# Optimization experiments

Measured on AMD Instinct MI355X. Metric: run time of the kernel, lower is better.

Reference implementation:

```python
import jax, jax.numpy as jnp
import numpy as np

N_NODES = 100_000
N_EDGES = 1_000_000
IN_FTS = 64
EDGE_IN_FTS = 64
OUT_DIM = 64
LN_EPS = 1e-5


def setup_inputs() -> dict:
    key = jax.random.key(0)
    ks = jax.random.split(key, 9)
    def lin(k, fan_in, fan_out):
        bound = 1.0 / np.sqrt(fan_in)
        kw, kb = jax.random.split(k)
        W = jax.random.uniform(kw, (fan_out, fan_in), jnp.float32, -bound, bound)
        b = jax.random.uniform(kb, (fan_out,), jnp.float32, -bound, bound)
        return W, b
    node_fts = jax.random.normal(ks[0], (N_NODES, IN_FTS), jnp.float32)
    edge_fts = jax.random.normal(ks[1], (N_EDGES, EDGE_IN_FTS), jnp.float32)
    edges = jax.random.randint(ks[2], (2, N_EDGES), 0, N_NODES, jnp.int64)
    W_init, b_init = lin(ks[3], EDGE_IN_FTS, OUT_DIM)
    W_mlp, b_mlp = lin(ks[4], 2 * IN_FTS + OUT_DIM, OUT_DIM)
    W_alpha, b_alpha = lin(ks[5], 2 * IN_FTS + OUT_DIM, 1)
    return {
        "node_fts": node_fts, "edge_fts": edge_fts, "edges": edges,
        "W_init": W_init, "b_init": b_init,
        "W_mlp": W_mlp, "b_mlp": b_mlp,
        "W_alpha": W_alpha, "b_alpha": b_alpha,
    }


def _layer_norm(x):
    # F.layer_norm over last dim, no affine params
    m = jnp.mean(x, axis=-1, keepdims=True)
    v = jnp.mean(jnp.square(x - m), axis=-1, keepdims=True)
    return (x - m) * jax.lax.rsqrt(v + LN_EPS)


def reference(node_fts, edge_fts, edges, W_init, b_init, W_mlp, b_mlp, W_alpha, b_alpha):
    # initial edge projection: [E, edge_in] -> [E, out_dim]
    e = edge_fts @ W_init.T + b_init
    # gather head/tail node features: [E, in_fts] each
    head_vectors = jnp.take(node_fts, edges[0], axis=0)
    tail_vectors = jnp.take(node_fts, edges[1], axis=0)
    combined = jnp.concatenate([e, head_vectors, tail_vectors], axis=1)  # [E, 2*in+out]
    alpha = jax.nn.sigmoid(combined @ W_alpha.T + b_alpha)  # [E, 1]
    processed = jnp.tanh(combined @ W_mlp.T + b_mlp)        # [E, out_dim]
    right_side = _layer_norm(processed) * alpha
    return _layer_norm(e + right_side)
```

## Files before the change

kernel.cpp:

```cpp
#include <hip/hip_runtime.h>
#include <hip/hip_bf16.h>

typedef __bf16 bf16;
typedef bf16 bf16x8 __attribute__((ext_vector_type(8)));
typedef float f32x4 __attribute__((ext_vector_type(4)));

#define MFMA16(a, b, c) __builtin_amdgcn_mfma_f32_16x16x32_bf16((a), (b), (c), 0, 0, 0)
#define UNROLL _Pragma("unroll")

__device__ __forceinline__ float fast_rcp(float x) { return __builtin_amdgcn_rcpf(x); }
__device__ __forceinline__ float fast_rsq(float x) { return __builtin_amdgcn_rsqf(x); }
__device__ __forceinline__ float fast_tanh(float x) {
    float e = __expf(2.0f * x);
    return 1.0f - 2.0f * fast_rcp(e + 1.0f);
}
__device__ __forceinline__ float fast_sigmoid(float x) {
    return fast_rcp(1.0f + __expf(-x));
}

__device__ __forceinline__ bf16x8 cvt8(const float* __restrict__ p) {
    f32x4 a = *(const f32x4*)p;
    f32x4 b = *(const f32x4*)(p + 4);
    bf16x8 r;
    r[0] = (bf16)a[0]; r[1] = (bf16)a[1]; r[2] = (bf16)a[2]; r[3] = (bf16)a[3];
    r[4] = (bf16)b[0]; r[5] = (bf16)b[1]; r[6] = (bf16)b[2]; r[7] = (bf16)b[3];
    return r;
}
__device__ __forceinline__ bf16x8 cvt8v(f32x4 a, f32x4 b) {
    bf16x8 r;
    r[0] = (bf16)a[0]; r[1] = (bf16)a[1]; r[2] = (bf16)a[2]; r[3] = (bf16)a[3];
    r[4] = (bf16)b[0]; r[5] = (bf16)b[1]; r[6] = (bf16)b[2]; r[7] = (bf16)b[3];
    return r;
}

template <int CTRL>
__device__ __forceinline__ float dpp_add(float v) {
    int t = __builtin_amdgcn_update_dpp(0, __float_as_int(v), CTRL, 0xF, 0xF, false);
    return v + __int_as_float(t);
}
__device__ __forceinline__ float sum16(float v) {
    v = dpp_add<0x121>(v);
    v = dpp_add<0x122>(v);
    v = dpp_add<0x124>(v);
    v = dpp_add<0x128>(v);
    return v;
}

#define WS_WAF  8192
#define WS_BMF  8320
#define WS_BAF  8576
#define WS_NODE 16384

__global__ void prep_kernel(const float* __restrict__ W_init,
                            const float* __restrict__ b_init,
                            const float* __restrict__ W_mlp,
                            const float* __restrict__ b_mlp,
                            const float* __restrict__ W_alpha,
                            const float* __restrict__ b_alpha,
                            const float* __restrict__ node_fts,
                            char* __restrict__ ws,
                            int nchunks)
{
    const int idx = blockIdx.x * 256 + threadIdx.x;
    if (blockIdx.x < 17) {
        bf16*  Wf  = (bf16*)ws;
        bf16*  waf = (bf16*)(ws + WS_WAF);
        float* bMf = (float*)(ws + WS_BMF);
        float* bAf = (float*)(ws + WS_BAF);
        if (idx < 4096) {
            const int o = idx >> 6, k = idx & 63;
            float acc = 0.f;
            for (int j = 0; j < 64; ++j)
                acc += W_mlp[o * 192 + j] * W_init[j * 64 + k];
            Wf[o * 64 + k] = (bf16)acc;
        } else if (idx < 4160) {
            const int o = idx - 4096;
            float acc = b_mlp[o];
            for (int j = 0; j < 64; ++j)
                acc += W_mlp[o * 192 + j] * b_init[j];
            bMf[o] = acc;
        } else if (idx < 4224) {
            const int k = idx - 4160;
            float acc = 0.f;
            for (int j = 0; j < 64; ++j)
                acc += W_alpha[j] * W_init[j * 64 + k];
            waf[k] = (bf16)acc;
        } else if (idx == 4224) {
            float acc = b_alpha[0];
            for (int j = 0; j < 64; ++j)
                acc += W_alpha[j] * b_init[j];
            bAf[0] = acc;
        }
    } else {
        const int i = idx - 17 * 256;
        if (i < nchunks) {
            bf16* nc = (bf16*)(ws + WS_NODE);
            f32x4 a = *(const f32x4*)(node_fts + (size_t)i * 8);
            f32x4 b = *(const f32x4*)(node_fts + (size_t)i * 8 + 4);
            *(bf16x8*)(nc + (size_t)i * 8) = cvt8v(a, b);
        }
    }
}

#define ISSUE_STAGE(sp, e0s, hs, ts)                                          \
    {                                                                         \
        const float* ep_ = edge_fts + ((size_t)(e0s) + n) * 64;               \
        ef[sp][0] = *(const f32x4*)(ep_ + q * 8);                             \
        ef[sp][1] = *(const f32x4*)(ep_ + q * 8 + 4);                         \
        ef[sp][2] = *(const f32x4*)(ep_ + 32 + q * 8);                        \
        ef[sp][3] = *(const f32x4*)(ep_ + 32 + q * 8 + 4);                    \
        if constexpr (NB) {                                                   \
            const bf16* hp_ = nc + (size_t)(hs) * 64;                         \
            const bf16* tp_ = nc + (size_t)(ts) * 64;                         \
            nhB[sp][0] = *(const bf16x8*)(hp_ + q * 8);                       \
            nhB[sp][1] = *(const bf16x8*)(hp_ + 32 + q * 8);                  \
            ntB[sp][0] = *(const bf16x8*)(tp_ + q * 8);                       \
            ntB[sp][1] = *(const bf16x8*)(tp_ + 32 + q * 8);                  \
        } else {                                                              \
            const float* hp_ = node_fts + (size_t)(hs) * 64;                  \
            const float* tp_ = node_fts + (size_t)(ts) * 64;                  \
            nhF[sp][0] = *(const f32x4*)(hp_ + q * 8);                        \
            nhF[sp][1] = *(const f32x4*)(hp_ + q * 8 + 4);                    \
            nhF[sp][2] = *(const f32x4*)(hp_ + 32 + q * 8);                   \
            nhF[sp][3] = *(const f32x4*)(hp_ + 32 + q * 8 + 4);               \
            ntF[sp][0] = *(const f32x4*)(tp_ + q * 8);                        \
            ntF[sp][1] = *(const f32x4*)(tp_ + q * 8 + 4);                    \
            ntF[sp][2] = *(const f32x4*)(tp_ + 32 + q * 8);                   \
            ntF[sp][3] = *(const f32x4*)(tp_ + 32 + q * 8 + 4);               \
        }                                                                     \
    }

template <bool NB>
__global__ __launch_bounds__(256, 3)
void edge_update_kernel(const float* __restrict__ node_fts,
                        const float* __restrict__ edge_fts,
                        const int*   __restrict__ edges,
                        const float* __restrict__ W_init,
                        const float* __restrict__ b_init,
                        const float* __restrict__ W_mlp,
                        const float* __restrict__ W_alpha,
                        const char*  __restrict__ ws,
                        float* __restrict__ out,
                        int E)
{
    __shared__ bf16 sW2[64][264];
    __shared__ bf16 sWa[224];

    const int tid  = threadIdx.x;
    const int lane = tid & 63;
    const int wv   = tid >> 6;
    const int n    = lane & 15;
    const int q    = lane >> 4;

    const bf16*  Wf  = (const bf16*)ws;
    const bf16*  waf = (const bf16*)(ws + WS_WAF);
    const float* bMf = (const float*)(ws + WS_BMF);
    const float* bAf = (const float*)(ws + WS_BAF);
    const bf16*  nc  = (const bf16*)(ws + WS_NODE);

    for (int c = tid; c < 64 * 33; c += 256) {
        const int r = c / 33;
        const int o = (c - r * 33) * 8;
        if (o < 64)       *(bf16x8*)(&sW2[r][o]) = *(const bf16x8*)(Wf + r * 64 + o);
        else if (o < 192) *(bf16x8*)(&sW2[r][o]) = cvt8(W_mlp + r * 192 + o);
        else if (o < 256) *(bf16x8*)(&sW2[r][o]) = cvt8(W_init + r * 64 + (o - 192));
    }
    if (tid < 24) {
        const int o = tid * 8;
        if (o < 64) *(bf16x8*)(&sWa[o]) = *(const bf16x8*)(waf + o);
        else        *(bf16x8*)(&sWa[o]) = cvt8(W_alpha + o);
    }
    __syncthreads();

    float bI[4], bM[4];
    UNROLL
    for (int t = 0; t < 4; ++t) {
        bI[t] = b_init[t * 16 + n];
        bM[t] = bMf[t * 16 + n];
    }
    const float bA = bAf[0];

    const int ngroups = E >> 4;
    const int stride  = gridDim.x * 4;
    int gc = blockIdx.x * 4 + wv;
    if (gc >= ngroups) return;

    f32x4  ef[2][4];
    bf16x8 nhB[2][2], ntB[2][2];
    f32x4  nhF[2][4], ntF[2][4];

    {
        const int e0 = gc << 4;
        const int hc = edges[e0 + n];
        const int tc = edges[E + e0 + n];
        ISSUE_STAGE(0, e0, hc, tc);
    }
    int gn = gc + stride, hn = 0, tn = 0;
    if (gn < ngroups) {
        const int e0n = gn << 4;
        hn = edges[e0n + n];
        tn = edges[E + e0n + n];
    } else {
        gn = gc;
    }

    for (;;) {
        UNROLL
        for (int p = 0; p < 2; ++p) {
            const int np = p ^ 1;
            const bool haveNext = (gn != gc);
            int g2 = gn;
            if (haveNext) {
                ISSUE_STAGE(np, gn << 4, hn, tn);
                g2 = gn + stride;
                if (g2 < ngroups) {
                    const int e2 = g2 << 4;
                    hn = edges[e2 + n];
                    tn = edges[E + e2 + n];
                } else {
                    g2 = gn;
                }
            }

            const int e0c = gc << 4;
            bf16x8 A[6];
            A[0] = cvt8v(ef[p][0], ef[p][1]);
            A[1] = cvt8v(ef[p][2], ef[p][3]);
            if constexpr (NB) {
                A[2] = nhB[p][0]; A[3] = nhB[p][1];
                A[4] = ntB[p][0]; A[5] = ntB[p][1];
            } else {
                A[2] = cvt8v(nhF[p][0], nhF[p][1]); A[3] = cvt8v(nhF[p][2], nhF[p][3]);
                A[4] = cvt8v(ntF[p][0], ntF[p][1]); A[5] = cvt8v(ntF[p][2], ntF[p][3]);
            }

            f32x4 accE[4] = { f32x4{0,0,0,0}, f32x4{0,0,0,0}, f32x4{0,0,0,0}, f32x4{0,0,0,0} };
            UNROLL
            for (int kk = 0; kk < 2; ++kk)
                UNROLL
                for (int t = 0; t < 4; ++t)
                    accE[t] = MFMA16(A[kk],
                                     *(const bf16x8*)(&sW2[t * 16 + n][192 + kk * 32 + q * 8]),
                                     accE[t]);

            f32x4 accP[4] = { f32x4{0,0,0,0}, f32x4{0,0,0,0}, f32x4{0,0,0,0}, f32x4{0,0,0,0} };
            f32x4 accA = f32x4{0,0,0,0};
            UNROLL
            for (int kk = 0; kk < 6; ++kk) {
                accA = MFMA16(A[kk], *(const bf16x8*)(&sWa[kk * 32 + q * 8]), accA);
                UNROLL
                for (int t = 0; t < 4; ++t)
                    accP[t] = MFMA16(A[kk],
                                     *(const bf16x8*)(&sW2[t * 16 + n][kk * 32 + q * 8]),
                                     accP[t]);
            }

            float eF[4][4], pv[4][4], alpha[4];
            UNROLL
            for (int t = 0; t < 4; ++t)
                UNROLL
                for (int r = 0; r < 4; ++r) eF[t][r] = accE[t][r] + bI[t];
            UNROLL
            for (int r = 0; r < 4; ++r) alpha[r] = fast_sigmoid(accA[r] + bA);
            UNROLL
            for (int t = 0; t < 4; ++t)
                UNROLL
                for (int r = 0; r < 4; ++r) pv[t][r] = fast_tanh(accP[t][r] + bM[t]);

            float s1[4], s2[4];
            UNROLL
            for (int r = 0; r < 4; ++r) {
                s1[r] = pv[0][r] + pv[1][r] + pv[2][r] + pv[3][r];
                s2[r] = pv[0][r]*pv[0][r] + pv[1][r]*pv[1][r] + pv[2][r]*pv[2][r] + pv[3][r]*pv[3][r];
            }
            UNROLL
            for (int r = 0; r < 4; ++r) { s1[r] = sum16(s1[r]); s2[r] = sum16(s2[r]); }

            float o2[4][4];
            UNROLL
            for (int r = 0; r < 4; ++r) {
                const float mean = s1[r] * 0.015625f;
                const float var  = fmaxf(s2[r] * 0.015625f - mean * mean, 0.0f);
                const float rs   = fast_rsq(var + 1e-5f);
                UNROLL
                for (int t = 0; t < 4; ++t)
                    o2[t][r] = eF[t][r] + (pv[t][r] - mean) * rs * alpha[r];
            }

            UNROLL
            for (int r = 0; r < 4; ++r) {
                s1[r] = o2[0][r] + o2[1][r] + o2[2][r] + o2[3][r];
                s2[r] = o2[0][r]*o2[0][r] + o2[1][r]*o2[1][r] + o2[2][r]*o2[2][r] + o2[3][r]*o2[3][r];
            }
            UNROLL
            for (int r = 0; r < 4; ++r) { s1[r] = sum16(s1[r]); s2[r] = sum16(s2[r]); }

            UNROLL
            for (int r = 0; r < 4; ++r) {
                const float mean = s1[r] * 0.015625f;
                const float var  = fmaxf(s2[r] * 0.015625f - mean * mean, 0.0f);
                const float rs   = fast_rsq(var + 1e-5f);
                UNROLL
                for (int t = 0; t < 4; ++t)
                    out[((size_t)e0c + q * 4 + r) * 64 + t * 16 + n] = (o2[t][r] - mean) * rs;
            }

            if (!haveNext) return;
            gc = gn;
            gn = g2;
        }
    }
}

extern "C" void kernel_launch(void* const* d_in, const int* in_sizes, int n_in,
                              void* d_out, int out_size, void* d_ws, size_t ws_size,
                              hipStream_t stream) {
    const float* node_fts = (const float*)d_in[0];
    const float* edge_fts = (const float*)d_in[1];
    const int*   edges    = (const int*)d_in[2];
    const float* W_init   = (const float*)d_in[3];
    const float* b_init   = (const float*)d_in[4];
    const float* W_mlp    = (const float*)d_in[5];
    const float* b_mlp    = (const float*)d_in[6];
    const float* W_alpha  = (const float*)d_in[7];
    const float* b_alpha  = (const float*)d_in[8];
    float* out = (float*)d_out;
    char*  ws  = (char*)d_ws;

    const int E = in_sizes[2] / 2;
    const int N = in_sizes[0] / 64;

    const size_t need = (size_t)WS_NODE + (size_t)N * 64 * 2;
    const bool   nb   = ws_size >= need;
    const int    nchunks = N * 8;

    const int prep_blocks = nb ? (17 + (nchunks + 255) / 256) : 17;
    hipLaunchKernelGGL(prep_kernel, dim3(prep_blocks), dim3(256), 0, stream,
                       W_init, b_init, W_mlp, b_mlp, W_alpha, b_alpha,
                       node_fts, ws, nb ? nchunks : 0);

    if (nb) {
        hipLaunchKernelGGL((edge_update_kernel<true>), dim3(2048), dim3(256), 0, stream,
                           node_fts, edge_fts, edges, W_init, b_init,
                           W_mlp, W_alpha, ws, out, E);
    } else {
        hipLaunchKernelGGL((edge_update_kernel<false>), dim3(2048), dim3(256), 0, stream,
                           node_fts, edge_fts, edges, W_init, b_init,
                           W_mlp, W_alpha, ws, out, E);
    }
}
```

Measured before the change: 695.3 us.

## Stage bf16 node cache in output tail, drop double-buffered prefetch loop

The bf16 node-feature cache now lives in the tail of the output buffer instead of the workspace. The main kernel processes all groups except that tail, and a second small launch then computes the tail edges from fp32 node features, overwriting the cache. The software double-buffered prefetch loop is replaced by a simple grid-stride loop. Edge features and node features are read with nontemporal loads, and the W_init MFMA operands are held in registers instead of LDS, which shrinks the shared tile. The trade is less explicit latency hiding and an extra launch, in exchange for a cache that no longer depends on workspace size, lower register pressure and less LDS.

```diff
diff --git a/kernel.cpp b/kernel.cpp
--- a/kernel.cpp
+++ b/kernel.cpp
@@ -16,6 +16,10 @@
 }
 __device__ __forceinline__ float fast_sigmoid(float x) {
     return fast_rcp(1.0f + __expf(-x));
+}
+
+__device__ __forceinline__ f32x4 ldnt4(const float* __restrict__ p) {
+    return __builtin_nontemporal_load((const f32x4*)p);
 }
 
 __device__ __forceinline__ bf16x8 cvt8(const float* __restrict__ p) {
@@ -49,7 +53,6 @@
 #define WS_WAF  8192
 #define WS_BMF  8320
 #define WS_BAF  8576
-#define WS_NODE 16384
 
 __global__ void prep_kernel(const float* __restrict__ W_init,
                             const float* __restrict__ b_init,
@@ -59,6 +62,7 @@
                             const float* __restrict__ b_alpha,
                             const float* __restrict__ node_fts,
                             char* __restrict__ ws,
+                            bf16* __restrict__ ncache,
                             int nchunks)
 {
     const int idx = blockIdx.x * 256 + threadIdx.x;
@@ -94,41 +98,12 @@
     } else {
         const int i = idx - 17 * 256;
         if (i < nchunks) {
-            bf16* nc = (bf16*)(ws + WS_NODE);
-            f32x4 a = *(const f32x4*)(node_fts + (size_t)i * 8);
-            f32x4 b = *(const f32x4*)(node_fts + (size_t)i * 8 + 4);
-            *(bf16x8*)(nc + (size_t)i * 8) = cvt8v(a, b);
-        }
-    }
-}
-
-#define ISSUE_STAGE(sp, e0s, hs, ts)                                          \
-    {                                                                         \
-        const float* ep_ = edge_fts + ((size_t)(e0s) + n) * 64;               \
-        ef[sp][0] = *(const f32x4*)(ep_ + q * 8);                             \
-        ef[sp][1] = *(const f32x4*)(ep_ + q * 8 + 4);                         \
-        ef[sp][2] = *(const f32x4*)(ep_ + 32 + q * 8);                        \
-        ef[sp][3] = *(const f32x4*)(ep_ + 32 + q * 8 + 4);                    \
-        if constexpr (NB) {                                                   \
-            const bf16* hp_ = nc + (size_t)(hs) * 64;                         \
-            const bf16* tp_ = nc + (size_t)(ts) * 64;                         \
-            nhB[sp][0] = *(const bf16x8*)(hp_ + q * 8);                       \
-            nhB[sp][1] = *(const bf16x8*)(hp_ + 32 + q * 8);                  \
-            ntB[sp][0] = *(const bf16x8*)(tp_ + q * 8);                       \
-            ntB[sp][1] = *(const bf16x8*)(tp_ + 32 + q * 8);                  \
-        } else {                                                              \
-            const float* hp_ = node_fts + (size_t)(hs) * 64;                  \
-            const float* tp_ = node_fts + (size_t)(ts) * 64;                  \
-            nhF[sp][0] = *(const f32x4*)(hp_ + q * 8);                        \
-            nhF[sp][1] = *(const f32x4*)(hp_ + q * 8 + 4);                    \
-            nhF[sp][2] = *(const f32x4*)(hp_ + 32 + q * 8);                   \
-            nhF[sp][3] = *(const f32x4*)(hp_ + 32 + q * 8 + 4);               \
-            ntF[sp][0] = *(const f32x4*)(tp_ + q * 8);                        \
-            ntF[sp][1] = *(const f32x4*)(tp_ + q * 8 + 4);                    \
-            ntF[sp][2] = *(const f32x4*)(tp_ + 32 + q * 8);                   \
-            ntF[sp][3] = *(const f32x4*)(tp_ + 32 + q * 8 + 4);               \
-        }                                                                     \
-    }
+            f32x4 a = ldnt4(node_fts + (size_t)i * 8);
+            f32x4 b = ldnt4(node_fts + (size_t)i * 8 + 4);
+            *(bf16x8*)(ncache + (size_t)i * 8) = cvt8v(a, b);
+        }
+    }
+}
 
 template <bool NB>
 __global__ __launch_bounds__(256, 3)
@@ -140,10 +115,11 @@
                         const float* __restrict__ W_mlp,
                         const float* __restrict__ W_alpha,
                         const char*  __restrict__ ws,
+                        const bf16*  __restrict__ nc,
                         float* __restrict__ out,
-                        int E)
+                        int E, int g0, int g1)
 {
-    __shared__ bf16 sW2[64][264];
+    __shared__ bf16 sW2[64][200];
     __shared__ bf16 sWa[224];
 
     const int tid  = threadIdx.x;
@@ -156,14 +132,12 @@
     const bf16*  waf = (const bf16*)(ws + WS_WAF);
     const float* bMf = (const float*)(ws + WS_BMF);
     const float* bAf = (const float*)(ws + WS_BAF);
-    const bf16*  nc  = (const bf16*)(ws + WS_NODE);
-
-    for (int c = tid; c < 64 * 33; c += 256) {
-        const int r = c / 33;
-        const int o = (c - r * 33) * 8;
-        if (o < 64)       *(bf16x8*)(&sW2[r][o]) = *(const bf16x8*)(Wf + r * 64 + o);
-        else if (o < 192) *(bf16x8*)(&sW2[r][o]) = cvt8(W_mlp + r * 192 + o);
-        else if (o < 256) *(bf16x8*)(&sW2[r][o]) = cvt8(W_init + r * 64 + (o - 192));
+
+    for (int c = tid; c < 64 * 24; c += 256) {
+        const int r = c / 24;
+        const int o = (c - r * 24) * 8;
+        if (o < 64) *(bf16x8*)(&sW2[r][o]) = *(const bf16x8*)(Wf + r * 64 + o);
+        else        *(bf16x8*)(&sW2[r][o]) = cvt8(W_mlp + r * 192 + o);
     }
     if (tid < 24) {
         const int o = tid * 8;
@@ -171,6 +145,13 @@
         else        *(bf16x8*)(&sWa[o]) = cvt8(W_alpha + o);
     }
     __syncthreads();
+
+    bf16x8 B1[2][4];
+    UNROLL
+    for (int kk = 0; kk < 2; ++kk)
+        UNROLL
+        for (int t = 0; t < 4; ++t)
+            B1[kk][t] = cvt8(W_init + (t * 16 + n) * 64 + kk * 32 + q * 8);
 
     float bI[4], bM[4];
     UNROLL
@@ -180,134 +161,95 @@
     }
     const float bA = bAf[0];
 
-    const int ngroups = E >> 4;
-    const int stride  = gridDim.x * 4;
-    int gc = blockIdx.x * 4 + wv;
-    if (gc >= ngroups) return;
-
-    f32x4  ef[2][4];
-    bf16x8 nhB[2][2], ntB[2][2];
-    f32x4  nhF[2][4], ntF[2][4];
-
-    {
-        const int e0 = gc << 4;
-        const int hc = edges[e0 + n];
-        const int tc = edges[E + e0 + n];
-        ISSUE_STAGE(0, e0, hc, tc);
-    }
-    int gn = gc + stride, hn = 0, tn = 0;
-    if (gn < ngroups) {
-        const int e0n = gn << 4;
-        hn = edges[e0n + n];
-        tn = edges[E + e0n + n];
-    } else {
-        gn = gc;
-    }
-
-    for (;;) {
-        UNROLL
-        for (int p = 0; p < 2; ++p) {
-            const int np = p ^ 1;
-            const bool haveNext = (gn != gc);
-            int g2 = gn;
-            if (haveNext) {
-                ISSUE_STAGE(np, gn << 4, hn, tn);
-                g2 = gn + stride;
-                if (g2 < ngroups) {
-                    const int e2 = g2 << 4;
-                    hn = edges[e2 + n];
-                    tn = edges[E + e2 + n];
-                } else {
-                    g2 = gn;
-                }
-            }
-
-            const int e0c = gc << 4;
-            bf16x8 A[6];
-            A[0] = cvt8v(ef[p][0], ef[p][1]);
-            A[1] = cvt8v(ef[p][2], ef[p][3]);
-            if constexpr (NB) {
-                A[2] = nhB[p][0]; A[3] = nhB[p][1];
-                A[4] = ntB[p][0]; A[5] = ntB[p][1];
-            } else {
-                A[2] = cvt8v(nhF[p][0], nhF[p][1]); A[3] = cvt8v(nhF[p][2], nhF[p][3]);
-                A[4] = cvt8v(ntF[p][0], ntF[p][1]); A[5] = cvt8v(ntF[p][2], ntF[p][3]);
-            }
-
-            f32x4 accE[4] = { f32x4{0,0,0,0}, f32x4{0,0,0,0}, f32x4{0,0,0,0}, f32x4{0,0,0,0} };
-            UNROLL
-            for (int kk = 0; kk < 2; ++kk)
-                UNROLL
-                for (int t = 0; t < 4; ++t)
-                    accE[t] = MFMA16(A[kk],
-                                     *(const bf16x8*)(&sW2[t * 16 + n][192 + kk * 32 + q * 8]),
-                                     accE[t]);
-
-            f32x4 accP[4] = { f32x4{0,0,0,0}, f32x4{0,0,0,0}, f32x4{0,0,0,0}, f32x4{0,0,0,0} };
-            f32x4 accA = f32x4{0,0,0,0};
-            UNROLL
-            for (int kk = 0; kk < 6; ++kk) {
-                accA = MFMA16(A[kk], *(const bf16x8*)(&sWa[kk * 32 + q * 8]), accA);
-                UNROLL
-                for (int t = 0; t < 4; ++t)
-                    accP[t] = MFMA16(A[kk],
-                                     *(const bf16x8*)(&sW2[t * 16 + n][kk * 32 + q * 8]),
-                                     accP[t]);
-            }
-
-            float eF[4][4], pv[4][4], alpha[4];
+    for (int g = g0 + blockIdx.x * 4 + wv; g < g1; g += gridDim.x * 4) {
+        const int e0 = g << 4;
+        const int h  = edges[e0 + n];
+        const int tl = edges[E + e0 + n];
+
+        bf16x8 A[6];
+        const float* ep = edge_fts + (size_t)(e0 + n) * 64;
+        A[0] = cvt8v(ldnt4(ep + q * 8), ldnt4(ep + q * 8 + 4));
+        A[1] = cvt8v(ldnt4(ep + 32 + q * 8), ldnt4(ep + 32 + q * 8 + 4));
+        if constexpr (NB) {
+            const bf16* hp = nc + (size_t)h * 64;
+            const bf16* tp = nc + (size_t)tl * 64;
+            A[2] = *(const bf16x8*)(hp + q * 8);
+            A[3] = *(const bf16x8*)(hp + 32 + q * 8);
+            A[4] = *(const bf16x8*)(tp + q * 8);
+            A[5] = *(const bf16x8*)(tp + 32 + q * 8);
+        } else {
+            const float* hp = node_fts + (size_t)h * 64;
+            const float* tp = node_fts + (size_t)tl * 64;
+            A[2] = cvt8(hp + q * 8);
+            A[3] = cvt8(hp + 32 + q * 8);
+            A[4] = cvt8(tp + q * 8);
+            A[5] = cvt8(tp + 32 + q * 8);
+        }
+
+        f32x4 accE[4] = { f32x4{0,0,0,0}, f32x4{0,0,0,0}, f32x4{0,0,0,0}, f32x4{0,0,0,0} };
+        UNROLL
+        for (int kk = 0; kk < 2; ++kk)
+            UNROLL
+            for (int t = 0; t < 4; ++t) accE[t] = MFMA16(A[kk], B1[kk][t], accE[t]);
+
+        f32x4 accP[4] = { f32x4{0,0,0,0}, f32x4{0,0,0,0}, f32x4{0,0,0,0}, f32x4{0,0,0,0} };
+        f32x4 accA = f32x4{0,0,0,0};
+        UNROLL
+        for (int kk = 0; kk < 6; ++kk) {
+            accA = MFMA16(A[kk], *(const bf16x8*)(&sWa[kk * 32 + q * 8]), accA);
             UNROLL
             for (int t = 0; t < 4; ++t)
-                UNROLL
-                for (int r = 0; r < 4; ++r) eF[t][r] = accE[t][r] + bI[t];
-            UNROLL
-            for (int r = 0; r < 4; ++r) alpha[r] = fast_sigmoid(accA[r] + bA);
+                accP[t] = MFMA16(A[kk], *(const bf16x8*)(&sW2[t * 16 + n][kk * 32 + q * 8]), accP[t]);
+        }
+
+        float eF[4][4], pv[4][4], alpha[4];
+        UNROLL
+        for (int t = 0; t < 4; ++t)
+            UNROLL
+            for (int r = 0; r < 4; ++r) eF[t][r] = accE[t][r] + bI[t];
+        UNROLL
+        for (int r = 0; r < 4; ++r) alpha[r] = fast_sigmoid(accA[r] + bA);
+        UNROLL
+        for (int t = 0; t < 4; ++t)
+            UNROLL
+            for (int r = 0; r < 4; ++r) pv[t][r] = fast_tanh(accP[t][r] + bM[t]);
+
+        float s1[4], s2[4];
+        UNROLL
+        for (int r = 0; r < 4; ++r) {
+            s1[r] = pv[0][r] + pv[1][r] + pv[2][r] + pv[3][r];
+            s2[r] = pv[0][r]*pv[0][r] + pv[1][r]*pv[1][r] + pv[2][r]*pv[2][r] + pv[3][r]*pv[3][r];
+        }
+        UNROLL
+        for (int r = 0; r < 4; ++r) { s1[r] = sum16(s1[r]); s2[r] = sum16(s2[r]); }
+
+        float o2[4][4];
+        UNROLL
+        for (int r = 0; r < 4; ++r) {
+            const float mean = s1[r] * 0.015625f;
+            const float var  = fmaxf(s2[r] * 0.015625f - mean * mean, 0.0f);
+            const float rs   = fast_rsq(var + 1e-5f);
             UNROLL
             for (int t = 0; t < 4; ++t)
-                UNROLL
-                for (int r = 0; r < 4; ++r) pv[t][r] = fast_tanh(accP[t][r] + bM[t]);
-
-            float s1[4], s2[4];
-            UNROLL
-            for (int r = 0; r < 4; ++r) {
-                s1[r] = pv[0][r] + pv[1][r] + pv[2][r] + pv[3][r];
-                s2[r] = pv[0][r]*pv[0][r] + pv[1][r]*pv[1][r] + pv[2][r]*pv[2][r] + pv[3][r]*pv[3][r];
-            }
-            UNROLL
-            for (int r = 0; r < 4; ++r) { s1[r] = sum16(s1[r]); s2[r] = sum16(s2[r]); }
-
-            float o2[4][4];
-            UNROLL
-            for (int r = 0; r < 4; ++r) {
-                const float mean = s1[r] * 0.015625f;
-                const float var  = fmaxf(s2[r] * 0.015625f - mean * mean, 0.0f);
-                const float rs   = fast_rsq(var + 1e-5f);
-                UNROLL
-                for (int t = 0; t < 4; ++t)
-                    o2[t][r] = eF[t][r] + (pv[t][r] - mean) * rs * alpha[r];
-            }
-
-            UNROLL
-            for (int r = 0; r < 4; ++r) {
-                s1[r] = o2[0][r] + o2[1][r] + o2[2][r] + o2[3][r];
-                s2[r] = o2[0][r]*o2[0][r] + o2[1][r]*o2[1][r] + o2[2][r]*o2[2][r] + o2[3][r]*o2[3][r];
-            }
-            UNROLL
-            for (int r = 0; r < 4; ++r) { s1[r] = sum16(s1[r]); s2[r] = sum16(s2[r]); }
-
-            UNROLL
-            for (int r = 0; r < 4; ++r) {
-                const float mean = s1[r] * 0.015625f;
-                const float var  = fmaxf(s2[r] * 0.015625f - mean * mean, 0.0f);
-                const float rs   = fast_rsq(var + 1e-5f);
-                UNROLL
-                for (int t = 0; t < 4; ++t)
-                    out[((size_t)e0c + q * 4 + r) * 64 + t * 16 + n] = (o2[t][r] - mean) * rs;
-            }
-
-            if (!haveNext) return;
-            gc = gn;
-            gn = g2;
+                o2[t][r] = eF[t][r] + (pv[t][r] - mean) * rs * alpha[r];
+        }
+
+        UNROLL
+        for (int r = 0; r < 4; ++r) {
+            s1[r] = o2[0][r] + o2[1][r] + o2[2][r] + o2[3][r];
+            s2[r] = o2[0][r]*o2[0][r] + o2[1][r]*o2[1][r] + o2[2][r]*o2[2][r] + o2[3][r]*o2[3][r];
+        }
+        UNROLL
+        for (int r = 0; r < 4; ++r) { s1[r] = sum16(s1[r]); s2[r] = sum16(s2[r]); }
+
+        UNROLL
+        for (int r = 0; r < 4; ++r) {
+            const float mean = s1[r] * 0.015625f;
+            const float var  = fmaxf(s2[r] * 0.015625f - mean * mean, 0.0f);
+            const float rs   = fast_rsq(var + 1e-5f);
+            UNROLL
+            for (int t = 0; t < 4; ++t)
+                out[((size_t)e0 + q * 4 + r) * 64 + t * 16 + n] = (o2[t][r] - mean) * rs;
         }
     }
 }
@@ -329,23 +271,33 @@
 
     const int E = in_sizes[2] / 2;
     const int N = in_sizes[0] / 64;
-
-    const size_t need = (size_t)WS_NODE + (size_t)N * 64 * 2;
-    const bool   nb   = ws_size >= need;
-    const int    nchunks = N * 8;
-
-    const int prep_blocks = nb ? (17 + (nchunks + 255) / 256) : 17;
+    const int totalGroups = E >> 4;
+
+    int cacheRows = ((N + 1) / 2 + 15) & ~15;
+    cacheRows += (E - cacheRows) & 15;
+    const bool useCache = (E >= cacheRows + 16) && (cacheRows > 0);
+
+    bf16* ncache = useCache ? (bf16*)(out + (size_t)(E - cacheRows) * 64) : (bf16*)nullptr;
+    const int nchunks = useCache ? N * 8 : 0;
+
+    const int prep_blocks = 17 + (nchunks + 255) / 256;
     hipLaunchKernelGGL(prep_kernel, dim3(prep_blocks), dim3(256), 0, stream,
                        W_init, b_init, W_mlp, b_mlp, W_alpha, b_alpha,
-                       node_fts, ws, nb ? nchunks : 0);
-
-    if (nb) {
+                       node_fts, ws, ncache, nchunks);
+
+    if (useCache) {
+        const int mainGroups = (E - cacheRows) >> 4;
         hipLaunchKernelGGL((edge_update_kernel<true>), dim3(2048), dim3(256), 0, stream,
                            node_fts, edge_fts, edges, W_init, b_init,
-                           W_mlp, W_alpha, ws, out, E);
+                           W_mlp, W_alpha, ws, ncache, out, E, 0, mainGroups);
+        hipLaunchKernelGGL((edge_update_kernel<false>), dim3(256), dim3(256), 0, stream,
+                           node_fts, edge_fts, edges, W_init, b_init,
+                           W_mlp, W_alpha, ws, (const bf16*)nullptr, out, E,
+                           mainGroups, totalGroups);
     } else {
         hipLaunchKernelGGL((edge_update_kernel<false>), dim3(2048), dim3(256), 0, stream,
                            node_fts, edge_fts, edges, W_init, b_init,
-                           W_mlp, W_alpha, ws, out, E);
-    }
-}
+                           W_mlp, W_alpha, ws, (const bf16*)nullptr, out, E,
+                           0, totalGroups);
+    }
+}
```

Result: no change. 703.4 us (+1.2%).
